# Performance work log

Hardware: AMD Instinct MI355X
Metric: run time of the kernel (lower is better)

The kernel has to match this reference:

```python
import jax, jax.numpy as jnp
import numpy as np

N_HEADS = 8
N_HEAD_CH = 32
N_GROUPS = 8
NC = N_HEADS * N_HEAD_CH          # 256
GC = NC // N_GROUPS               # 32 group channels
OFFSET_RANGE_FACTOR = 2.0


def _layer_norm(x, w, b, eps=1e-5):
    mu = jnp.mean(x, -1, keepdims=True)
    var = jnp.var(x, -1, keepdims=True)
    return (x - mu) * jax.lax.rsqrt(var + eps) * w + b


def _conv2dmod(x, style, W):
    # StyleGAN2-style modulated 1x1 conv (lucidrains Conv2DMod, demod=True).
    # x (B,Ci,H,W), style (B,Ci), W (Co,Ci)
    w = W[None] * (style[:, None, :] + 1.0)                      # (B,Co,Ci)
    d = jax.lax.rsqrt(jnp.sum(w * w, axis=2, keepdims=True) + 1e-8)
    w = w * d
    return jnp.einsum('boi,bihw->bohw', w, x)


def _dwconv3x3(x, w, b):
    # depthwise 3x3, stride 1, pad 1; w (C,1,3,3)
    out = jax.lax.conv_general_dilated(
        x, w, window_strides=(1, 1), padding=[(1, 1), (1, 1)],
        dimension_numbers=('NCHW', 'OIHW', 'NCHW'),
        feature_group_count=x.shape[1])
    return out + b[None, :, None, None]


def _grid_sample(img, grid):
    # bilinear, align_corners=True, padding_mode='zeros'
    # img (N,C,H,W), grid (N,Hg,Wg,2) in xy order, values in ~[-1,1]
    N, C, H, W = img.shape
    gx = (grid[..., 0] + 1.0) * 0.5 * (W - 1)
    gy = (grid[..., 1] + 1.0) * 0.5 * (H - 1)
    x0 = jnp.floor(gx); y0 = jnp.floor(gy)
    wx1 = gx - x0; wy1 = gy - y0

    def gather(ix, iy):
        valid = ((ix >= 0) & (ix <= W - 1) & (iy >= 0) & (iy <= H - 1)).astype(img.dtype)
        ixc = jnp.clip(ix, 0, W - 1).astype(jnp.int32)
        iyc = jnp.clip(iy, 0, H - 1).astype(jnp.int32)
        vals = jax.vmap(lambda im, yy, xx: im[:, yy, xx])(img, iyc, ixc)  # (N,C,Hg,Wg)
        return vals * valid[:, None]

    x1 = x0 + 1.0; y1 = y0 + 1.0
    return (gather(x0, y0) * ((1 - wx1) * (1 - wy1))[:, None]
            + gather(x1, y0) * (wx1 * (1 - wy1))[:, None]
            + gather(x0, y1) * ((1 - wx1) * wy1)[:, None]
            + gather(x1, y1) * (wx1 * wy1)[:, None])


def _ref_points(Hk, Wk, BG, dtype):
    ry = jnp.linspace(0.5, Hk - 0.5, Hk, dtype=dtype) / (Hk - 1.0) * 2.0 - 1.0
    rx = jnp.linspace(0.5, Wk - 0.5, Wk, dtype=dtype) / (Wk - 1.0) * 2.0 - 1.0
    ref = jnp.stack(jnp.meshgrid(ry, rx, indexing='ij'), -1)  # (Hk,Wk,2) yx
    return jnp.broadcast_to(ref[None], (BG, Hk, Wk, 2))


def setup_inputs() -> dict:
    key = jax.random.key(0)
    ks = jax.random.split(key, 16)
    s = 0.02
    inp = {
        'x': jax.random.normal(ks[0], (2, NC, 32, 32), jnp.float32),
        'q': jax.random.normal(ks[1], (8, 2048, NC), jnp.float32),
        'mask': (jax.random.uniform(ks[2], (8, 2048, 1)) > 0.2).astype(jnp.float32),
        'Wq': jax.random.normal(ks[3], (NC, NC), jnp.float32) * s,
        'bq': jnp.zeros((NC,), jnp.float32),
        'Wmod': jax.random.normal(ks[4], (NC, NC), jnp.float32),
        'dw_w': jax.random.normal(ks[5], (GC, 1, 3, 3), jnp.float32) * s,
        'dw_b': jnp.zeros((GC,), jnp.float32),
        'ln_w': jnp.ones((GC,), jnp.float32),
        'ln_b': jnp.zeros((GC,), jnp.float32),
        'off_w': jax.random.normal(ks[6], (2, GC), jnp.float32) * s,
        'Wk': jax.random.normal(ks[7], (NC, NC), jnp.float32) * s,
        'bk': jnp.zeros((NC,), jnp.float32),
        'Wv': jax.random.normal(ks[8], (NC, NC), jnp.float32) * s,
        'bv': jnp.zeros((NC,), jnp.float32),
        'Wo': jax.random.normal(ks[9], (NC, NC), jnp.float32) * s,
        'bo': jnp.zeros((NC,), jnp.float32),
    }
    return inp


def reference(x, q, mask, Wq, bq, Wmod, dw_w, dw_b, ln_w, ln_b, off_w,
              Wk, bk, Wv, bv, Wo, bo):
    rn = q.shape[0] // x.shape[0]
    B, L, C = q.shape
    H, W = x.shape[2], x.shape[3]

    # masked mean pooling of queries -> conditioning vector
    q_cond = jnp.sum(q * mask, axis=1) / (jnp.sum(mask, axis=1) + 1e-6)   # (B,C)
    q_cond = q_cond @ Wq.T + bq

    # tile reference features: 'ref_n c h w -> (rn ref_n) c h w'
    xr = jnp.tile(x, (rn, 1, 1, 1))                                       # (B,C,H,W)

    # modulated 1x1 conv, then per-group offset network
    q_t = _conv2dmod(xr, q_cond, Wmod)                                    # (B,C,H,W)
    q_off = q_t.reshape(B * N_GROUPS, GC, H, W)
    t = _dwconv3x3(q_off, dw_w, dw_b)
    t = jnp.transpose(t, (0, 2, 3, 1))
    t = _layer_norm(t, ln_w, ln_b)
    t = jax.nn.gelu(t, approximate=False)
    t = jnp.transpose(t, (0, 3, 1, 2))
    offset = jnp.einsum('oi,bihw->bohw', off_w, t)                        # (BG,2,Hk,Wk)

    Hk, Wk_ = offset.shape[2], offset.shape[3]
    n_sample = Hk * Wk_
    offset_range = jnp.array([1.0 / (Hk - 1.0), 1.0 / (Wk_ - 1.0)],
                             dtype=x.dtype).reshape(1, 2, 1, 1)
    offset = jnp.tanh(offset) * offset_range * OFFSET_RANGE_FACTOR
    offset = jnp.transpose(offset, (0, 2, 3, 1))                          # (BG,Hk,Wk,2) yx

    ref = _ref_points(Hk, Wk_, B * N_GROUPS, x.dtype)
    pos = offset + ref                                                    # no clamp (orf>=0)

    # deformable gather
    xs = _grid_sample(xr.reshape(B * N_GROUPS, GC, H, W), pos[..., ::-1]) # (BG,GC,Hk,Wk)
    xs = xs.reshape(B, C, 1, n_sample)

    k = (jnp.einsum('oi,bimn->bomn', Wk, xs) + bk[None, :, None, None]
         ).reshape(B * N_HEADS, N_HEAD_CH, n_sample)
    v = (jnp.einsum('oi,bimn->bomn', Wv, xs) + bv[None, :, None, None]
         ).reshape(B * N_HEADS, N_HEAD_CH, n_sample)
    qh = jnp.transpose(q, (0, 2, 1)).reshape(B * N_HEADS, N_HEAD_CH, L)

    scale = N_HEAD_CH ** (-0.5)
    attn = jnp.einsum('bcm,bcn->bmn', qh, k) * scale                      # (BH,L,ns)
    # NOTE: source's attn.masked_fill(...) is non-in-place and discarded -> no mask here
    attn = jax.nn.softmax(attn, axis=2)
    out = jnp.einsum('bmn,bcn->bcm', attn, v)                             # (BH,hc,L)

    # '(b gn) c l -> b l (gn c)' with gn = n_groups (== n_heads)
    out = out.reshape(B, N_GROUPS, N_HEAD_CH, L).transpose(0, 3, 1, 2).reshape(B, L, NC)
    y = out @ Wo.T + bo
    return (y,
            pos.reshape(B, N_GROUPS, Hk, Wk_, 2),
            ref.reshape(B, N_GROUPS, Hk, Wk_, 2))
```

## Files before the change

### kernel.cpp

```cpp
#include <hip/hip_runtime.h>
#include <math.h>

typedef unsigned int uint;
typedef unsigned short ushort;
typedef __attribute__((ext_vector_type(8))) short short8;
typedef __attribute__((ext_vector_type(4))) float f32x4;

constexpr int CB  = 8;
constexpr int CL  = 2048;
constexpr int CC  = 256;
constexpr int CHC = 32;
constexpr int CGC = 32;
constexpr int CHW = 1024;
constexpr int CNS = 1024;
constexpr int CBG = 64;

constexpr size_t WS_QCOND = 2176;
constexpr size_t WS_WMOD  = 4224;
constexpr size_t WS_XT    = 266368;
constexpr size_t WS_QT    = 528512;
constexpr size_t WS_XST   = 2756736;
constexpr size_t WS_KB    = 3805312;
constexpr size_t WS_VB    = 4853888;
constexpr size_t WS_WB    = 5902464;
constexpr size_t WS_TMPB  = 6000768;
constexpr size_t WS_QB    = 8097920;
constexpr size_t WS_PART  = 10195072;
constexpr size_t WS_MPART = 10260608;

static __device__ __forceinline__ ushort f2bf(float f) {
  uint u = __float_as_uint(f);
  return (ushort)((u + 0x7FFFu + ((u >> 16) & 1u)) >> 16);
}
static __device__ __forceinline__ float bf2f(ushort u) {
  return __uint_as_float((uint)u << 16);
}
static __device__ __forceinline__ uint pack2bf(float a, float b) {
  return (uint)f2bf(a) | ((uint)f2bf(b) << 16);
}
static __device__ __forceinline__ uint packtrunc(float lo, float hi) {
  return __builtin_amdgcn_perm(__float_as_uint(hi), __float_as_uint(lo), 0x07060302u);
}

__global__ void k_poolprep(const float* __restrict__ q, const float* __restrict__ mask,
                           float* __restrict__ part, float* __restrict__ mpart,
                           ushort* __restrict__ qb,
                           const float* __restrict__ x, const float* __restrict__ Wk,
                           const float* __restrict__ Wv, const float* __restrict__ Wo,
                           ushort* __restrict__ xt, ushort* __restrict__ wb) {
  int bid = blockIdx.x;
  int tid = threadIdx.x;
  __shared__ float shbuf[64 * 65];
  if (bid < 256) {
    int b  = bid >> 5;
    int lc = bid & 31;
    int l0 = lc * 64;
    const float scale = 0.17677669529663687f * 1.4426950408889634f;
    float* mloc = shbuf;
    if (tid < 64) mloc[tid] = mask[b * CL + l0 + tid];
    __syncthreads();
    if (tid == 0) {
      float s = 0.f;
      for (int j = 0; j < 64; j++) s += mloc[j];
      mpart[b * 32 + lc] = s;
    }
    float acc = 0.f;
    const float* qp = q + (size_t)(b * CL + l0) * CC + tid;
    ushort* qw = qb + (size_t)(b * CL + l0) * CC + tid;
    for (int j = 0; j < 64; j++) {
      float v = qp[(size_t)j * CC];
      acc += v * mloc[j];
      qw[(size_t)j * CC] = f2bf(v * scale);
    }
    part[((size_t)(b * 32 + lc)) * CC + tid] = acc;
  } else if (bid < 384) {
    int b2 = bid - 256;
    int ref  = b2 >> 6;
    int cblk = (b2 >> 4) & 3;
    int hwblk = b2 & 15;
    float (*t)[65] = (float(*)[65])shbuf;
    int c0 = cblk * 64, hw0 = hwblk * 64;
    const float* src = x + (size_t)ref * CC * CHW;
    int hl = tid & 63, cq = tid >> 6;
    #pragma unroll
    for (int r = 0; r < 16; r++) {
      int cl = cq * 16 + r;
      t[cl][hl] = src[(size_t)(c0 + cl) * CHW + hw0 + hl];
    }
    __syncthreads();
    int cl2 = tid & 63, hq = tid >> 6;
    #pragma unroll
    for (int r = 0; r < 16; r++) {
      int hwl = hq * 16 + r;
      xt[((size_t)(ref * CHW + hw0 + hwl)) * CC + c0 + cl2] = f2bf(t[cl2][hwl]);
    }
  } else {
    int t2 = (bid - 384) * 256 + tid;
    int which = t2 >> 13;
    size_t off = ((size_t)(t2 & 8191)) * 8;
    const float* src = (which == 0) ? Wk : (which == 1) ? Wv : Wo;
    float4 a = *(const float4*)(src + off);
    float4 b = *(const float4*)(src + off + 4);
    uint4 r;
    r.x = pack2bf(a.x, a.y); r.y = pack2bf(a.z, a.w);
    r.z = pack2bf(b.x, b.y); r.w = pack2bf(b.z, b.w);
    *(uint4*)(wb + (size_t)which * 65536 + off) = r;
  }
}

__global__ void k_qcond(const float* __restrict__ part, const float* __restrict__ mpart,
                        const float* __restrict__ Wq, const float* __restrict__ bq,
                        float* __restrict__ qcond) {
  int b = blockIdx.x, o = threadIdx.x;
  __shared__ float qm[CC];
  __shared__ float ms;
  float s = 0.f;
  const float* pp = part + (size_t)b * 32 * CC + o;
  #pragma unroll
  for (int lc = 0; lc < 32; lc++) s += pp[(size_t)lc * CC];
  if (o < 32) {
    float m = mpart[b * 32 + o];
    #pragma unroll
    for (int k = 1; k < 32; k <<= 1) m += __shfl_xor(m, k, 32);
    if (o == 0) ms = m;
  }
  __syncthreads();
  float inv = 1.f / (ms + 1e-6f);
  qm[o] = s * inv;
  __syncthreads();
  float acc = bq[o];
  const float* wrow = Wq + (size_t)o * CC;
  for (int i = 0; i < CC; i++) acc += wrow[i] * qm[i];
  qcond[b * CC + o] = acc;
}

__global__ void k_wprep(const float* __restrict__ Wmod, const float* __restrict__ qcond,
                        ushort* __restrict__ wmodb) {
  int b  = blockIdx.x >> 4;
  int og = blockIdx.x & 15;
  int tid = threadIdx.x;
  int ol = tid >> 4, seg = tid & 15;
  int o = og * 16 + ol;
  const float* wr = Wmod + (size_t)o * CC + seg * 16;
  const float* qc = qcond + b * CC + seg * 16;
  float m[16];
  float ss = 0.f;
  #pragma unroll
  for (int j = 0; j < 16; j++) {
    float v = wr[j] * (qc[j] + 1.f);
    m[j] = v;
    ss += v * v;
  }
  #pragma unroll
  for (int k = 1; k < 16; k <<= 1) ss += __shfl_xor(ss, k, 16);
  float d = rsqrtf(ss + 1e-8f);
  uint u[8];
  #pragma unroll
  for (int j = 0; j < 8; j++) u[j] = pack2bf(m[2 * j] * d, m[2 * j + 1] * d);
  ushort* dst = wmodb + ((size_t)(b * CC + o)) * CC + seg * 16;
  *(uint4*)(dst)     = make_uint4(u[0], u[1], u[2], u[3]);
  *(uint4*)(dst + 8) = make_uint4(u[4], u[5], u[6], u[7]);
}

__launch_bounds__(256)
__global__ void k_mod_mfma(const ushort* __restrict__ wmodb, const ushort* __restrict__ xt,
                           ushort* __restrict__ qtb) {
  int tid = threadIdx.x;
  int wid = tid >> 6, lane = tid & 63;
  int widx = blockIdx.x * 4 + wid;
  int b   = widx >> 10;
  int ot  = (widx >> 6) & 15;
  int hwt = widx & 63;
  int col = lane & 15, g = lane >> 4;
  int O0 = ot * 16, HW0 = hwt * 16;
  const ushort* ap = wmodb + ((size_t)(b * CC + O0 + col)) * CC + g * 8;
  const ushort* bp = xt + ((size_t)((b & 1) * CHW + HW0 + col)) * CC + g * 8;
  f32x4 acc = {0.f, 0.f, 0.f, 0.f};
  #pragma unroll
  for (int ks = 0; ks < 8; ks++) {
    short8 af = *(const short8*)(ap + ks * 32);
    short8 bf = *(const short8*)(bp + ks * 32);
    acc = __builtin_amdgcn_mfma_f32_16x16x32_bf16(af, bf, acc, 0, 0, 0);
  }
  uint2 st;
  st.x = pack2bf(acc[0], acc[1]);
  st.y = pack2bf(acc[2], acc[3]);
  *(uint2*)(qtb + ((size_t)(b * CHW + HW0 + col)) * CC + O0 + g * 4) = st;
}

__global__ void k_off_sample(const ushort* __restrict__ qtb, const float* __restrict__ dww,
                             const float* __restrict__ dwb, const float* __restrict__ lnw,
                             const float* __restrict__ lnb, const float* __restrict__ offw,
                             const ushort* __restrict__ xt,
                             float* __restrict__ out_pos, float* __restrict__ out_ref,
                             ushort* __restrict__ xst) {
  int bg   = blockIdx.x >> 7;
  int pblk = blockIdx.x & 127;
  int tid  = threadIdx.x;
  int c = tid & 31, pp = tid >> 5;
  int p0 = pblk * 8;
  int yy = p0 >> 5;
  int xx = (p0 & 31) + pp;
  int p  = p0 + pp;
  const ushort* src = qtb + ((size_t)(bg >> 3) * CHW) * CC + (bg & 7) * CGC + c;
  float acc = dwb[c];
  #pragma unroll
  for (int ky = 0; ky < 3; ky++) {
    int yr = yy + ky - 1;
    if (yr < 0 || yr > 31) continue;
    #pragma unroll
    for (int kx = 0; kx < 3; kx++) {
      int xc = xx + kx - 1;
      if (xc < 0 || xc > 31) continue;
      acc += dww[c * 9 + ky * 3 + kx] * bf2f(src[(size_t)(yr * 32 + xc) * CC]);
    }
  }
  float s1 = acc, s2 = acc * acc;
  #pragma unroll
  for (int m = 1; m < 32; m <<= 1) { s1 += __shfl_xor(s1, m, 32); s2 += __shfl_xor(s2, m, 32); }
  float mu  = s1 * (1.f / 32.f);
  float var = s2 * (1.f / 32.f) - mu * mu;
  float tn  = (acc - mu) * rsqrtf(var + 1e-5f) * lnw[c] + lnb[c];
  float g   = 0.5f * tn * (1.f + erff(tn * 0.70710678118654752f));
  float sy = offw[c] * g, sx = offw[32 + c] * g;
  #pragma unroll
  for (int m = 1; m < 32; m <<= 1) { sy += __shfl_xor(sy, m, 32); sx += __shfl_xor(sx, m, 32); }

  float mine  = tanhf((c & 1) ? sx : sy);
  float other = __shfl_xor(mine, 1, 32);
  float ty = (c & 1) ? other : mine;
  float tx = (c & 1) ? mine : other;

  float refy = (0.5f + (float)yy) * (2.f / 31.f) - 1.f;
  float refx = (0.5f + (float)xx) * (2.f / 31.f) - 1.f;
  float py = ty * (2.f / 31.f) + refy;
  float px = tx * (2.f / 31.f) + refx;
  if (c < 2) {
    int oidx = bg * 2048 + p * 2 + c;
    out_pos[oidx] = (c == 0) ? py : px;
    out_ref[oidx] = (c == 0) ? refy : refx;
  }

  float gx = (px + 1.f) * 15.5f;
  float gy = (py + 1.f) * 15.5f;
  float x0f = floorf(gx), y0f = floorf(gy);
  float wx = gx - x0f, wy = gy - y0f;
  int ix0 = (int)x0f, iy0 = (int)y0f;
  const ushort* img = xt + (size_t)(((bg >> 3) & 1)) * CHW * CC + (bg & 7) * CGC + c;
  float sacc = 0.f;
  #pragma unroll
  for (int dy = 0; dy < 2; dy++) {
    int iy = iy0 + dy;
    if (iy < 0 || iy > 31) continue;
    float wyv = dy ? wy : 1.f - wy;
    #pragma unroll
    for (int dx = 0; dx < 2; dx++) {
      int ix = ix0 + dx;
      if (ix < 0 || ix > 31) continue;
      float wxv = dx ? wx : 1.f - wx;
      sacc += wyv * wxv * bf2f(img[(size_t)(iy * 32 + ix) * CC]);
    }
  }
  xst[((size_t)((bg >> 3) * CNS) + p) * CC + (bg & 7) * CGC + c] = f2bf(sacc);
}

__launch_bounds__(256)
__global__ void k_kv_mfma(const ushort* __restrict__ xst, const ushort* __restrict__ wkb,
                          const ushort* __restrict__ wvb, const float* __restrict__ bk,
                          const float* __restrict__ bv, ushort* __restrict__ kb,
                          ushort* __restrict__ vb) {
  int tid = threadIdx.x;
  int wid = tid >> 6, lane = tid & 63;
  int widx = blockIdx.x * 4 + wid;
  int b   = widx >> 8;
  int ntg = (widx >> 3) & 31;
  int otg = widx & 7;
  int col = lane & 15, g = lane >> 4;
  int N0 = ntg * 32, O0 = otg * 32;

  const ushort* xs0 = xst + ((size_t)(b * CNS + N0 + col)) * CC + g * 8;
  const ushort* xs1 = xs0 + (size_t)16 * CC;
  const ushort* wk0 = wkb + (size_t)(O0 + col) * CC + g * 8;
  const ushort* wk1 = wk0 + (size_t)16 * CC;
  const ushort* wv0 = wvb + (size_t)(O0 + col) * CC + g * 8;
  const ushort* wv1 = wv0 + (size_t)16 * CC;

  f32x4 ka[2][2], va[2][2];
  #pragma unroll
  for (int Y = 0; Y < 2; Y++) {
    float bvv = bv[O0 + Y * 16 + col];
    #pragma unroll
    for (int r = 0; r < 4; r++) {
      float bkv = bk[O0 + Y * 16 + g * 4 + r];
      ka[0][Y][r] = bkv; ka[1][Y][r] = bkv;
      va[0][Y][r] = bvv; va[1][Y][r] = bvv;
    }
  }

  #pragma unroll
  for (int ks = 0; ks < 8; ks++) {
    short8 xf0 = *(const short8*)(xs0 + ks * 32);
    short8 xf1 = *(const short8*)(xs1 + ks * 32);
    short8 kf0 = *(const short8*)(wk0 + ks * 32);
    short8 kf1 = *(const short8*)(wk1 + ks * 32);
    short8 vf0 = *(const short8*)(wv0 + ks * 32);
    short8 vf1 = *(const short8*)(wv1 + ks * 32);
    ka[0][0] = __builtin_amdgcn_mfma_f32_16x16x32_bf16(kf0, xf0, ka[0][0], 0, 0, 0);
    ka[0][1] = __builtin_amdgcn_mfma_f32_16x16x32_bf16(kf1, xf0, ka[0][1], 0, 0, 0);
    ka[1][0] = __builtin_amdgcn_mfma_f32_16x16x32_bf16(kf0, xf1, ka[1][0], 0, 0, 0);
    ka[1][1] = __builtin_amdgcn_mfma_f32_16x16x32_bf16(kf1, xf1, ka[1][1], 0, 0, 0);
    va[0][0] = __builtin_amdgcn_mfma_f32_16x16x32_bf16(xf0, vf0, va[0][0], 0, 0, 0);
    va[0][1] = __builtin_amdgcn_mfma_f32_16x16x32_bf16(xf0, vf1, va[0][1], 0, 0, 0);
    va[1][0] = __builtin_amdgcn_mfma_f32_16x16x32_bf16(xf1, vf0, va[1][0], 0, 0, 0);
    va[1][1] = __builtin_amdgcn_mfma_f32_16x16x32_bf16(xf1, vf1, va[1][1], 0, 0, 0);
  }

  #pragma unroll
  for (int X = 0; X < 2; X++)
    #pragma unroll
    for (int Y = 0; Y < 2; Y++) {
      int Oy = O0 + Y * 16, Nx = N0 + X * 16;
      {
        int hh = Oy >> 5;
        int c0 = (Oy & 31) + g * 4;
        uint2 w;
        w.x = pack2bf(ka[X][Y][0], ka[X][Y][1]);
        w.y = pack2bf(ka[X][Y][2], ka[X][Y][3]);
        *(uint2*)(kb + ((size_t)((b * 8 + hh) * CNS + Nx + col)) * CHC + c0) = w;
      }
      {
        int o = Oy + col;
        int hh = o >> 5;
        uint2 w;
        w.x = pack2bf(va[X][Y][0], va[X][Y][1]);
        w.y = pack2bf(va[X][Y][2], va[X][Y][3]);
        *(uint2*)(vb + ((size_t)((b * 8 + hh) * CHC + (o & 31))) * CNS + Nx + g * 4) = w;
      }
    }
}

__launch_bounds__(512, 4)
__global__ void k_attn_mfma(const ushort* __restrict__ qb, const ushort* __restrict__ kb,
                            const ushort* __restrict__ vb, ushort* __restrict__ tmpb) {
  int bh = blockIdx.x >> 3;
  int mb = blockIdx.x & 7;
  int b = bh >> 3, h = bh & 7;
  int tid = threadIdx.x;
  int wid = tid >> 6, lane = tid & 63;
  int col = lane & 15, g = lane >> 4;
  int mA = mb * 256 + wid * 32 + col;

  __shared__ ushort Kst[2][2][64 * 40];
  __shared__ ushort Vst[2][2][32 * 72];
  __shared__ ushort plds[8][2048];

  char* pwA = (char*)&plds[wid][0];
  char* pwB = (char*)&plds[wid][1024];
  int swz = (col & 7) << 4;
  int wb0 = col * 128 + g * 8;
  int rb0 = (col * 128 + g * 16) ^ swz;
  int rb1 = (col * 128 + 64 + g * 16) ^ swz;

  const ushort* qpA = qb + ((size_t)(b * CL + mA)) * CC + h * CHC + g * 8;
  short8 qfA = *(const short8*)qpA;
  short8 qfB = *(const short8*)(qpA + 16 * CC);

  const ushort* kglob = kb + (size_t)bh * 32768 + tid * 4;
  const ushort* vglob = vb + (size_t)bh * 32768 + (tid >> 4) * 1024 + (tid & 15) * 4;
  int kdst = (tid >> 3) * 40 + (tid & 7) * 4;
  int vdst = (tid >> 4) * 72 + (tid & 15) * 4;

  f32x4 oA0 = {0.f,0.f,0.f,0.f}, oA1 = {0.f,0.f,0.f,0.f};
  f32x4 oB0 = {0.f,0.f,0.f,0.f}, oB1 = {0.f,0.f,0.f,0.f};
  float lA = 0.f, lB = 0.f;

  {
    uint2 k0 = *(const uint2*)(kglob);
    uint2 k1 = *(const uint2*)(kglob + 2048);
    uint2 v0 = *(const uint2*)(vglob);
    uint2 v1 = *(const uint2*)(vglob + 64);
    *(uint2*)&Kst[0][0][kdst] = k0;
    *(uint2*)&Kst[0][1][kdst] = k1;
    *(uint2*)&Vst[0][0][vdst] = v0;
    *(uint2*)&Vst[0][1][vdst] = v1;
  }
  __syncthreads();

  int cur = 0;
  for (int it = 0; it < 8; it++) {
    uint2 kx0, kx1, vx0, vx1;
    if (it < 7) {
      int cb = (it + 1) * 2;
      kx0 = *(const uint2*)(kglob + (size_t)cb * 2048);
      kx1 = *(const uint2*)(kglob + (size_t)(cb + 1) * 2048);
      vx0 = *(const uint2*)(vglob + (size_t)cb * 64);
      vx1 = *(const uint2*)(vglob + (size_t)(cb + 1) * 64);
    }

    #pragma unroll
    for (int s = 0; s < 2; s++) {
      const ushort* Kc = &Kst[cur][s][0];
      const ushort* Vc = &Vst[cur][s][0];
      short8 kf0 = *(const short8*)(Kc + ( 0 + col) * 40 + g * 8);
      short8 kf1 = *(const short8*)(Kc + (16 + col) * 40 + g * 8);
      short8 kf2 = *(const short8*)(Kc + (32 + col) * 40 + g * 8);
      short8 kf3 = *(const short8*)(Kc + (48 + col) * 40 + g * 8);
      short8 vf00 = *(const short8*)(Vc + (col     ) * 72 +  0 + g * 8);
      short8 vf01 = *(const short8*)(Vc + (col     ) * 72 + 32 + g * 8);
      short8 vf10 = *(const short8*)(Vc + (col + 16) * 72 +  0 + g * 8);
      short8 vf11 = *(const short8*)(Vc + (col + 16) * 72 + 32 + g * 8);

      f32x4 zero = {0.f,0.f,0.f,0.f};
      f32x4 sA0 = __builtin_amdgcn_mfma_f32_16x16x32_bf16(kf0, qfA, zero, 0, 0, 0);
      f32x4 sA1 = __builtin_amdgcn_mfma_f32_16x16x32_bf16(kf1, qfA, zero, 0, 0, 0);
      f32x4 sA2 = __builtin_amdgcn_mfma_f32_16x16x32_bf16(kf2, qfA, zero, 0, 0, 0);
      f32x4 sA3 = __builtin_amdgcn_mfma_f32_16x16x32_bf16(kf3, qfA, zero, 0, 0, 0);
      f32x4 sB0 = __builtin_amdgcn_mfma_f32_16x16x32_bf16(kf0, qfB, zero, 0, 0, 0);
      f32x4 sB1 = __builtin_amdgcn_mfma_f32_16x16x32_bf16(kf1, qfB, zero, 0, 0, 0);
      f32x4 sB2 = __builtin_amdgcn_mfma_f32_16x16x32_bf16(kf2, qfB, zero, 0, 0, 0);
      f32x4 sB3 = __builtin_amdgcn_mfma_f32_16x16x32_bf16(kf3, qfB, zero, 0, 0, 0);

      {
        float ps = 0.f;
        #pragma unroll
        for (int f = 0; f < 4; f++) {
          f32x4 sv = (f == 0) ? sA0 : (f == 1) ? sA1 : (f == 2) ? sA2 : sA3;
          float p0 = __builtin_amdgcn_exp2f(sv[0]);
          float p1 = __builtin_amdgcn_exp2f(sv[1]);
          float p2 = __builtin_amdgcn_exp2f(sv[2]);
          float p3 = __builtin_amdgcn_exp2f(sv[3]);
          ps += (p0 + p1) + (p2 + p3);
          *(uint2*)(pwA + ((wb0 + f * 32) ^ swz)) = make_uint2(packtrunc(p0, p1), packtrunc(p2, p3));
        }
        lA += ps;
      }
      {
        float ps = 0.f;
        #pragma unroll
        for (int f = 0; f < 4; f++) {
          f32x4 sv = (f == 0) ? sB0 : (f == 1) ? sB1 : (f == 2) ? sB2 : sB3;
          float p0 = __builtin_amdgcn_exp2f(sv[0]);
          float p1 = __builtin_amdgcn_exp2f(sv[1]);
          float p2 = __builtin_amdgcn_exp2f(sv[2]);
          float p3 = __builtin_amdgcn_exp2f(sv[3]);
          ps += (p0 + p1) + (p2 + p3);
          *(uint2*)(pwB + ((wb0 + f * 32) ^ swz)) = make_uint2(packtrunc(p0, p1), packtrunc(p2, p3));
        }
        lB += ps;
      }

      short8 pfA0 = *(const short8*)(pwA + rb0);
      short8 pfA1 = *(const short8*)(pwA + rb1);
      short8 pfB0 = *(const short8*)(pwB + rb0);
      short8 pfB1 = *(const short8*)(pwB + rb1);

      oA0 = __builtin_amdgcn_mfma_f32_16x16x32_bf16(vf00, pfA0, oA0, 0, 0, 0);
      oA0 = __builtin_amdgcn_mfma_f32_16x16x32_bf16(vf01, pfA1, oA0, 0, 0, 0);
      oA1 = __builtin_amdgcn_mfma_f32_16x16x32_bf16(vf10, pfA0, oA1, 0, 0, 0);
      oA1 = __builtin_amdgcn_mfma_f32_16x16x32_bf16(vf11, pfA1, oA1, 0, 0, 0);
      oB0 = __builtin_amdgcn_mfma_f32_16x16x32_bf16(vf00, pfB0, oB0, 0, 0, 0);
      oB0 = __builtin_amdgcn_mfma_f32_16x16x32_bf16(vf01, pfB1, oB0, 0, 0, 0);
      oB1 = __builtin_amdgcn_mfma_f32_16x16x32_bf16(vf10, pfB0, oB1, 0, 0, 0);
      oB1 = __builtin_amdgcn_mfma_f32_16x16x32_bf16(vf11, pfB1, oB1, 0, 0, 0);
    }

    if (it < 7) {
      *(uint2*)&Kst[cur ^ 1][0][kdst] = kx0;
      *(uint2*)&Kst[cur ^ 1][1][kdst] = kx1;
      *(uint2*)&Vst[cur ^ 1][0][vdst] = vx0;
      *(uint2*)&Vst[cur ^ 1][1][vdst] = vx1;
    }
    __syncthreads();
    cur ^= 1;
  }

  lA += __shfl_xor(lA, 16); lA += __shfl_xor(lA, 32);
  lB += __shfl_xor(lB, 16); lB += __shfl_xor(lB, 32);
  float rlA = 1.f / lA, rlB = 1.f / lB;

  ushort* opA = tmpb + ((size_t)(b * CL + mA)) * CC + h * CHC;
  ushort* opB = opA + 16 * CC;
  {
    uint2 w0, w1;
    w0.x = pack2bf(oA0[0] * rlA, oA0[1] * rlA);
    w0.y = pack2bf(oA0[2] * rlA, oA0[3] * rlA);
    w1.x = pack2bf(oA1[0] * rlA, oA1[1] * rlA);
    w1.y = pack2bf(oA1[2] * rlA, oA1[3] * rlA);
    *(uint2*)(opA + g * 4) = w0;
    *(uint2*)(opA + 16 + g * 4) = w1;
  }
  {
    uint2 w0, w1;
    w0.x = pack2bf(oB0[0] * rlB, oB0[1] * rlB);
    w0.y = pack2bf(oB0[2] * rlB, oB0[3] * rlB);
    w1.x = pack2bf(oB1[0] * rlB, oB1[1] * rlB);
    w1.y = pack2bf(oB1[2] * rlB, oB1[3] * rlB);
    *(uint2*)(opB + g * 4) = w0;
    *(uint2*)(opB + 16 + g * 4) = w1;
  }
}

__launch_bounds__(256)
__global__ void k_yproj_mfma(const ushort* __restrict__ tmpb, const ushort* __restrict__ wob,
                             const float* __restrict__ bo, float* __restrict__ y) {
  int tid = threadIdx.x;
  int wid = tid >> 6, lane = tid & 63;
  int widx = blockIdx.x * 4 + wid;
  int rt2 = widx >> 1;
  int og = widx & 1;
  int col = lane & 15, g = lane >> 4;
  int R0 = rt2 * 32, O0 = og * 128;

  const ushort* ap0 = tmpb + ((size_t)(R0 + col)) * CC + g * 8;
  const ushort* ap1 = ap0 + (size_t)16 * CC;
  const ushort* bp = wob + (size_t)(O0 + col) * CC + g * 8;

  f32x4 acc[2][8];
  #pragma unroll
  for (int o4 = 0; o4 < 8; o4++) {
    float bb = bo[O0 + o4 * 16 + col];
    #pragma unroll
    for (int r = 0; r < 4; r++) { acc[0][o4][r] = bb; acc[1][o4][r] = bb; }
  }

  #pragma unroll
  for (int ks = 0; ks < 8; ks++) {
    short8 af0 = *(const short8*)(ap0 + ks * 32);
    short8 af1 = *(const short8*)(ap1 + ks * 32);
    #pragma unroll
    for (int o4 = 0; o4 < 8; o4++) {
      short8 bf = *(const short8*)(bp + (size_t)o4 * 16 * CC + ks * 32);
      acc[0][o4] = __builtin_amdgcn_mfma_f32_16x16x32_bf16(af0, bf, acc[0][o4], 0, 0, 0);
      acc[1][o4] = __builtin_amdgcn_mfma_f32_16x16x32_bf16(af1, bf, acc[1][o4], 0, 0, 0);
    }
  }

  #pragma unroll
  for (int rr = 0; rr < 2; rr++)
    #pragma unroll
    for (int o4 = 0; o4 < 8; o4++)
      #pragma unroll
      for (int r = 0; r < 4; r++)
        y[(size_t)(R0 + rr * 16 + g * 4 + r) * CC + O0 + o4 * 16 + col] = acc[rr][o4][r];
}

extern "C" void kernel_launch(void* const* d_in, const int* in_sizes, int n_in,
                              void* d_out, int out_size, void* d_ws, size_t ws_size,
                              hipStream_t stream) {
  const float* x    = (const float*)d_in[0];
  const float* q    = (const float*)d_in[1];
  const float* mask = (const float*)d_in[2];
  const float* Wq   = (const float*)d_in[3];
  const float* bq   = (const float*)d_in[4];
  const float* Wmod = (const float*)d_in[5];
  const float* dw_w = (const float*)d_in[6];
  const float* dw_b = (const float*)d_in[7];
  const float* ln_w = (const float*)d_in[8];
  const float* ln_b = (const float*)d_in[9];
  const float* offw = (const float*)d_in[10];
  const float* Wk   = (const float*)d_in[11];
  const float* bk   = (const float*)d_in[12];
  const float* Wv   = (const float*)d_in[13];
  const float* bv   = (const float*)d_in[14];
  const float* Wo   = (const float*)d_in[15];
  const float* bo   = (const float*)d_in[16];

  float* ws = (float*)d_ws;
  float* out = (float*)d_out;
  float* out_y   = out;
  float* out_pos = out + (size_t)CB * CL * CC;
  float* out_ref = out_pos + (size_t)CBG * CHW * 2;

  ushort* wmodb = (ushort*)(ws + WS_WMOD);
  ushort* xt    = (ushort*)(ws + WS_XT);
  ushort* qtb   = (ushort*)(ws + WS_QT);
  ushort* xst   = (ushort*)(ws + WS_XST);
  ushort* kbuf  = (ushort*)(ws + WS_KB);
  ushort* vbuf  = (ushort*)(ws + WS_VB);
  ushort* wkb   = (ushort*)(ws + WS_WB);
  ushort* wvb   = wkb + 65536;
  ushort* wob   = wkb + 131072;
  ushort* tmpb  = (ushort*)(ws + WS_TMPB);
  ushort* qbuf  = (ushort*)(ws + WS_QB);
  float*  part  = ws + WS_PART;
  float*  mpart = ws + WS_MPART;

  k_poolprep<<<480, 256, 0, stream>>>(q, mask, part, mpart, qbuf, x, Wk, Wv, Wo, xt, wkb);
  k_qcond<<<8, 256, 0, stream>>>(part, mpart, Wq, bq, ws + WS_QCOND);
  k_wprep<<<128, 256, 0, stream>>>(Wmod, ws + WS_QCOND, wmodb);
  k_mod_mfma<<<2048, 256, 0, stream>>>(wmodb, xt, qtb);
  k_off_sample<<<8192, 256, 0, stream>>>(qtb, dw_w, dw_b, ln_w, ln_b, offw, xt,
                                         out_pos, out_ref, xst);
  k_kv_mfma<<<512, 256, 0, stream>>>(xst, wkb, wvb, bk, bv, kbuf, vbuf);
  k_attn_mfma<<<512, 512, 0, stream>>>(qbuf, kbuf, vbuf, tmpb);
  k_yproj_mfma<<<256, 256, 0, stream>>>(tmpb, wob, bo, out_y);
}
```

Before: 126.6 us.

## Fuse qcond into wprep and register-tile modulated conv MFMA 2x2

Merges the style-vector projection kernel into the weight modulation kernel, so each of the 128 blocks recomputes its batch's qcond into shared memory instead of relying on a separate launch and a global round trip. The modulated 1x1 conv MFMA kernel now computes a 32x32 output tile per wave with four accumulators, reusing A and B fragments, and launches 4x fewer blocks. The trade is 16x redundant Wq matvec work per batch, more registers per wave, and less parallelism in the conv kernel.

```diff
diff --git a/kernel.cpp b/kernel.cpp
--- a/kernel.cpp
+++ b/kernel.cpp
@@ -15,7 +15,6 @@
 constexpr int CNS = 1024;
 constexpr int CBG = 64;
 
-constexpr size_t WS_QCOND = 2176;
 constexpr size_t WS_WMOD  = 4224;
 constexpr size_t WS_XT    = 266368;
 constexpr size_t WS_QT    = 528512;
@@ -108,46 +107,43 @@
   }
 }
 
-__global__ void k_qcond(const float* __restrict__ part, const float* __restrict__ mpart,
+__global__ void k_wprep(const float* __restrict__ part, const float* __restrict__ mpart,
                         const float* __restrict__ Wq, const float* __restrict__ bq,
-                        float* __restrict__ qcond) {
-  int b = blockIdx.x, o = threadIdx.x;
-  __shared__ float qm[CC];
-  __shared__ float ms;
-  float s = 0.f;
-  const float* pp = part + (size_t)b * 32 * CC + o;
-  #pragma unroll
-  for (int lc = 0; lc < 32; lc++) s += pp[(size_t)lc * CC];
-  if (o < 32) {
-    float m = mpart[b * 32 + o];
-    #pragma unroll
-    for (int k = 1; k < 32; k <<= 1) m += __shfl_xor(m, k, 32);
-    if (o == 0) ms = m;
-  }
-  __syncthreads();
-  float inv = 1.f / (ms + 1e-6f);
-  qm[o] = s * inv;
-  __syncthreads();
-  float acc = bq[o];
-  const float* wrow = Wq + (size_t)o * CC;
-  for (int i = 0; i < CC; i++) acc += wrow[i] * qm[i];
-  qcond[b * CC + o] = acc;
-}
-
-__global__ void k_wprep(const float* __restrict__ Wmod, const float* __restrict__ qcond,
-                        ushort* __restrict__ wmodb) {
+                        const float* __restrict__ Wmod, ushort* __restrict__ wmodb) {
   int b  = blockIdx.x >> 4;
   int og = blockIdx.x & 15;
   int tid = threadIdx.x;
+  __shared__ float qm[CC];
+  __shared__ float qcond_s[CC];
+  __shared__ float msh;
+
+  float s = 0.f;
+  const float* pp = part + (size_t)b * 32 * CC + tid;
+  #pragma unroll
+  for (int lc = 0; lc < 32; lc++) s += pp[(size_t)lc * CC];
+  if (tid < 32) {
+    float m = mpart[b * 32 + tid];
+    #pragma unroll
+    for (int k = 1; k < 32; k <<= 1) m += __shfl_xor(m, k, 32);
+    if (tid == 0) msh = m;
+  }
+  __syncthreads();
+  qm[tid] = s * (1.f / (msh + 1e-6f));
+  __syncthreads();
+  float qc = bq[tid];
+  const float* wrow = Wq + (size_t)tid * CC;
+  for (int i = 0; i < CC; i++) qc += wrow[i] * qm[i];
+  qcond_s[tid] = qc;
+  __syncthreads();
+
   int ol = tid >> 4, seg = tid & 15;
   int o = og * 16 + ol;
   const float* wr = Wmod + (size_t)o * CC + seg * 16;
-  const float* qc = qcond + b * CC + seg * 16;
   float m[16];
   float ss = 0.f;
   #pragma unroll
   for (int j = 0; j < 16; j++) {
-    float v = wr[j] * (qc[j] + 1.f);
+    float v = wr[j] * (qcond_s[seg * 16 + j] + 1.f);
     m[j] = v;
     ss += v * v;
   }
@@ -168,24 +164,41 @@
   int tid = threadIdx.x;
   int wid = tid >> 6, lane = tid & 63;
   int widx = blockIdx.x * 4 + wid;
-  int b   = widx >> 10;
-  int ot  = (widx >> 6) & 15;
-  int hwt = widx & 63;
+  int b   = widx >> 8;
+  int og  = (widx >> 5) & 7;
+  int hg  = widx & 31;
   int col = lane & 15, g = lane >> 4;
-  int O0 = ot * 16, HW0 = hwt * 16;
-  const ushort* ap = wmodb + ((size_t)(b * CC + O0 + col)) * CC + g * 8;
-  const ushort* bp = xt + ((size_t)((b & 1) * CHW + HW0 + col)) * CC + g * 8;
-  f32x4 acc = {0.f, 0.f, 0.f, 0.f};
+  int O0 = og * 32, HW0 = hg * 32;
+  const ushort* ap0 = wmodb + ((size_t)(b * CC + O0 + col)) * CC + g * 8;
+  const ushort* ap1 = ap0 + (size_t)16 * CC;
+  const ushort* bp0 = xt + ((size_t)((b & 1) * CHW + HW0 + col)) * CC + g * 8;
+  const ushort* bp1 = bp0 + (size_t)16 * CC;
+  f32x4 acc[2][2];
+  #pragma unroll
+  for (int X = 0; X < 2; X++)
+    #pragma unroll
+    for (int Y = 0; Y < 2; Y++)
+      acc[X][Y] = (f32x4){0.f, 0.f, 0.f, 0.f};
   #pragma unroll
   for (int ks = 0; ks < 8; ks++) {
-    short8 af = *(const short8*)(ap + ks * 32);
-    short8 bf = *(const short8*)(bp + ks * 32);
-    acc = __builtin_amdgcn_mfma_f32_16x16x32_bf16(af, bf, acc, 0, 0, 0);
-  }
-  uint2 st;
-  st.x = pack2bf(acc[0], acc[1]);
-  st.y = pack2bf(acc[2], acc[3]);
-  *(uint2*)(qtb + ((size_t)(b * CHW + HW0 + col)) * CC + O0 + g * 4) = st;
+    short8 af0 = *(const short8*)(ap0 + ks * 32);
+    short8 af1 = *(const short8*)(ap1 + ks * 32);
+    short8 bf0 = *(const short8*)(bp0 + ks * 32);
+    short8 bf1 = *(const short8*)(bp1 + ks * 32);
+    acc[0][0] = __builtin_amdgcn_mfma_f32_16x16x32_bf16(af0, bf0, acc[0][0], 0, 0, 0);
+    acc[0][1] = __builtin_amdgcn_mfma_f32_16x16x32_bf16(af0, bf1, acc[0][1], 0, 0, 0);
+    acc[1][0] = __builtin_amdgcn_mfma_f32_16x16x32_bf16(af1, bf0, acc[1][0], 0, 0, 0);
+    acc[1][1] = __builtin_amdgcn_mfma_f32_16x16x32_bf16(af1, bf1, acc[1][1], 0, 0, 0);
+  }
+  #pragma unroll
+  for (int X = 0; X < 2; X++)
+    #pragma unroll
+    for (int Y = 0; Y < 2; Y++) {
+      uint2 st;
+      st.x = pack2bf(acc[X][Y][0], acc[X][Y][1]);
+      st.y = pack2bf(acc[X][Y][2], acc[X][Y][3]);
+      *(uint2*)(qtb + ((size_t)(b * CHW + HW0 + Y * 16 + col)) * CC + O0 + X * 16 + g * 4) = st;
+    }
 }
 
 __global__ void k_off_sample(const ushort* __restrict__ qtb, const float* __restrict__ dww,
@@ -586,9 +599,8 @@
   float*  mpart = ws + WS_MPART;
 
   k_poolprep<<<480, 256, 0, stream>>>(q, mask, part, mpart, qbuf, x, Wk, Wv, Wo, xt, wkb);
-  k_qcond<<<8, 256, 0, stream>>>(part, mpart, Wq, bq, ws + WS_QCOND);
-  k_wprep<<<128, 256, 0, stream>>>(Wmod, ws + WS_QCOND, wmodb);
-  k_mod_mfma<<<2048, 256, 0, stream>>>(wmodb, xt, qtb);
+  k_wprep<<<128, 256, 0, stream>>>(part, mpart, Wq, bq, Wmod, wmodb);
+  k_mod_mfma<<<512, 256, 0, stream>>>(wmodb, xt, qtb);
   k_off_sample<<<8192, 256, 0, stream>>>(qtb, dw_w, dw_b, ln_w, ln_b, offw, xt,
                                          out_pos, out_ref, xst);
   k_kv_mfma<<<512, 256, 0, stream>>>(xst, wkb, wvb, bk, bv, kbuf, vbuf);
```

New measurement: 118.7 us (median of 3 runs). 6.2% less time.
